# Performance work log

Hardware: AMD Instinct MI355X
Metric: run time of the kernel (lower is better)

## Reference

```python
import jax, jax.numpy as jnp
import numpy as np

N = 50000      # nodes
E = 1600000    # edges (avg degree 32)
D_IN = 128
H = 256        # 2 * out_channels
D_OUT = 128
NEG_SLOPE = 0.2


def setup_inputs() -> dict:
    key = jax.random.key(0)
    ks = jax.random.split(key, 16)
    x = jax.random.normal(ks[0], (N, D_IN), dtype=jnp.float32)
    edge_index = jax.random.randint(ks[1], (2, E), 0, N, dtype=jnp.int64)

    def lin(k, fan_in, fan_out):
        s = 1.0 / np.sqrt(fan_in)
        return jax.random.uniform(k, (fan_in, fan_out), jnp.float32, -s, s)

    def att(k, d):
        s = 1.0 / np.sqrt(d)
        return jax.random.uniform(k, (d,), jnp.float32, -s, s)

    return {
        "x": x, "edge_index": edge_index,
        "W1": lin(ks[2], D_IN, H), "a1_src": att(ks[3], H), "a1_dst": att(ks[4], H), "b1": jnp.zeros((H,), jnp.float32),
        "W2": lin(ks[5], H, H),    "a2_src": att(ks[6], H), "a2_dst": att(ks[7], H), "b2": jnp.zeros((H,), jnp.float32),
        "W3": lin(ks[8], H, D_OUT),"a3_src": att(ks[9], D_OUT), "a3_dst": att(ks[10], D_OUT), "b3": jnp.zeros((D_OUT,), jnp.float32),
    }


def _gat_conv(x, W, a_src, a_dst, b, src, dst):
    # x: [N, Cin] -> h: [N, Cout]
    h = x @ W
    # per-node attention logits, gathered along edges (edge j->i: src=j, dst=i)
    e = jax.nn.leaky_relu((h @ a_src)[src] + (h @ a_dst)[dst], NEG_SLOPE)  # [E]
    # segment softmax over incoming edges of each destination node
    m = jax.ops.segment_max(e, dst, num_segments=N)          # [N]
    p = jnp.exp(e - m[dst])                                  # [E]
    denom = jax.ops.segment_sum(p, dst, num_segments=N)      # [N]
    alpha = p / denom[dst]                                   # [E]
    # scatter-add weighted source features
    out = jax.ops.segment_sum(alpha[:, None] * h[src], dst, num_segments=N)
    return out + b


def reference(x, edge_index, W1, a1_src, a1_dst, b1, W2, a2_src, a2_dst, b2, W3, a3_src, a3_dst, b3):
    src, dst = edge_index[0], edge_index[1]
    h = jax.nn.relu(_gat_conv(x, W1, a1_src, a1_dst, b1, src, dst))
    for _ in range(2):  # hidden_layers, shared conv2 weights
        h = jax.nn.relu(_gat_conv(h, W2, a2_src, a2_dst, b2, src, dst))
    out = _gat_conv(h, W3, a3_src, a3_dst, b3, src, dst)
    return jax.nn.softmax(out, axis=1)
```

## Files before the change

kernel.cpp:

```cpp
#include <hip/hip_runtime.h>
#include <hip/hip_bf16.h>
#include <hip/hip_fp16.h>

#define NN 50000
#define EE 1600000
#define DIN 128
#define HH 256
#define DOUT 128

typedef __attribute__((ext_vector_type(8))) short short8;
typedef __attribute__((ext_vector_type(4))) float f32x4;

__device__ __forceinline__ short f2bf(float v) {
    union { float f; unsigned u; } a;
    a.f = v;
    unsigned r = a.u + 0x7fffu + ((a.u >> 16) & 1u);
    return (short)(r >> 16);
}
__device__ __forceinline__ float bf2f(short h) {
    union { unsigned u; float f; } a;
    a.u = ((unsigned)(unsigned short)h) << 16;
    return a.f;
}


__global__ __launch_bounds__(256) void hist_kernel(const int* __restrict__ dst, int* __restrict__ deg, int E) {
    int e = blockIdx.x * 256 + threadIdx.x;
    if (e < E) atomicAdd(&deg[dst[e]], 1);
}

#define SCAN_B 256

__global__ __launch_bounds__(SCAN_B) void scan1_kernel(const int* __restrict__ deg, int* __restrict__ exc,
                                                       int* __restrict__ bsum, int n) {
    __shared__ int tmp[SCAN_B];
    int i = blockIdx.x * SCAN_B + threadIdx.x;
    int v = (i < n) ? deg[i] : 0;
    tmp[threadIdx.x] = v;
    __syncthreads();
    for (int o = 1; o < SCAN_B; o <<= 1) {
        int t = (threadIdx.x >= o) ? tmp[threadIdx.x - o] : 0;
        __syncthreads();
        tmp[threadIdx.x] += t;
        __syncthreads();
    }
    if (i < n) exc[i] = tmp[threadIdx.x] - v;
    if (threadIdx.x == SCAN_B - 1) bsum[blockIdx.x] = tmp[SCAN_B - 1];
}

__global__ __launch_bounds__(SCAN_B) void scan2_kernel(int* __restrict__ bsum, int nb) {
    __shared__ int tmp[SCAN_B];
    int v = (threadIdx.x < nb) ? bsum[threadIdx.x] : 0;
    tmp[threadIdx.x] = v;
    __syncthreads();
    for (int o = 1; o < SCAN_B; o <<= 1) {
        int t = (threadIdx.x >= o) ? tmp[threadIdx.x - o] : 0;
        __syncthreads();
        tmp[threadIdx.x] += t;
        __syncthreads();
    }
    if (threadIdx.x < nb) bsum[threadIdx.x] = tmp[threadIdx.x] - v;
}

__global__ __launch_bounds__(SCAN_B) void scan3_kernel(int* __restrict__ exc, const int* __restrict__ bsum,
                                                       int* __restrict__ cursor, int n, int E) {
    int i = blockIdx.x * SCAN_B + threadIdx.x;
    if (i < n) {
        int v = exc[i] + bsum[blockIdx.x];
        exc[i] = v;
        cursor[i] = v;
    }
    if (i == n) exc[n] = E;
}

#define NCB 256

__global__ __launch_bounds__(256) void scatter8_kernel(const int* __restrict__ src, const int* __restrict__ dst,
                                                       int* __restrict__ cursor, int* __restrict__ es, int E, int n) {
    int q = blockIdx.x & 7;
    int cb = blockIdx.x >> 3;
    int lo = q * (n >> 3);
    int hi = (q == 7) ? n : lo + (n >> 3);
    int chunk = (E + NCB - 1) / NCB;
    int e1 = min((cb + 1) * chunk, E);
    for (int e = cb * chunk + threadIdx.x; e < e1; e += 256) {
        int d = dst[e];
        if (d >= lo && d < hi) {
            int pos = atomicAdd(&cursor[d], 1);
            es[pos] = src[e];
        }
    }
}


__global__ __launch_bounds__(256) void wsplit_kernel(const float* __restrict__ W, short* __restrict__ WhT,
                                                     short* __restrict__ WlT, int K, int C) {
    int f = blockIdx.x * 256 + threadIdx.x;
    if (f >= K * C) return;
    int k = f / C, c = f % C;
    float v = W[f];
    short h = f2bf(v);
    short l = f2bf(v - bf2f(h));
    WhT[(size_t)c * K + k] = h;
    WlT[(size_t)c * K + k] = l;
}


__global__ __launch_bounds__(256) void tohalf_kernel(const float* __restrict__ in, __half* __restrict__ out,
                                                     size_t cnt) {
    size_t i = (size_t)(blockIdx.x * 256 + threadIdx.x) * 4;
    if (i + 3 < cnt) {
        float4 v = *(const float4*)(in + i);
        __half h0 = __float2half(v.x), h1 = __float2half(v.y);
        __half h2 = __float2half(v.z), h3 = __float2half(v.w);
        __half2* op = (__half2*)(out + i);
        op[0] = __half2(h0, h1);
        op[1] = __half2(h2, h3);
    }
}


template <bool BRELU, bool DOTS, bool HOUT>
__global__ __launch_bounds__(256) void gemm_mfma_kernel(const float* __restrict__ X, const short* __restrict__ BhT,
                                                        const short* __restrict__ BlT, const float* __restrict__ bias,
                                                        float* __restrict__ out, const float* __restrict__ a1v,
                                                        const float* __restrict__ a2v, float* __restrict__ s1,
                                                        float* __restrict__ s2, int n, int K, int Cout) {
    __shared__ short Ah[128][40], Al[128][40];
    __shared__ short Bh[128][40], Bl[128][40];
    int tid = threadIdx.x;
    int row0 = blockIdx.y * 128, col0 = blockIdx.x * 128;
    int lane = tid & 63, wid = tid >> 6;
    int wr = (wid >> 1) * 64, wc = (wid & 1) * 64;

    f32x4 acc[4][4];
#pragma unroll
    for (int mi = 0; mi < 4; ++mi)
#pragma unroll
        for (int ni = 0; ni < 4; ++ni) acc[mi][ni] = 0.f;

    int srow = tid >> 1;
    int sk = (tid & 1) * 16;

    for (int k0 = 0; k0 < K; k0 += 32) {
        {
            float v[16];
            int gr = row0 + srow;
            if (gr < n) {
                const float* p = X + (size_t)gr * K + k0 + sk;
                float4 f0 = ((const float4*)p)[0];
                float4 f1 = ((const float4*)p)[1];
                float4 f2 = ((const float4*)p)[2];
                float4 f3 = ((const float4*)p)[3];
                v[0] = f0.x; v[1] = f0.y; v[2] = f0.z; v[3] = f0.w;
                v[4] = f1.x; v[5] = f1.y; v[6] = f1.z; v[7] = f1.w;
                v[8] = f2.x; v[9] = f2.y; v[10] = f2.z; v[11] = f2.w;
                v[12] = f3.x; v[13] = f3.y; v[14] = f3.z; v[15] = f3.w;
            } else {
#pragma unroll
                for (int j = 0; j < 16; ++j) v[j] = 0.f;
            }
            short8 h0, h1, l0, l1;
#pragma unroll
            for (int j = 0; j < 8; ++j) {
                short h = f2bf(v[j]);
                h0[j] = h;
                l0[j] = f2bf(v[j] - bf2f(h));
            }
#pragma unroll
            for (int j = 0; j < 8; ++j) {
                short h = f2bf(v[8 + j]);
                h1[j] = h;
                l1[j] = f2bf(v[8 + j] - bf2f(h));
            }
            *(short8*)&Ah[srow][sk] = h0;
            *(short8*)&Ah[srow][sk + 8] = h1;
            *(short8*)&Al[srow][sk] = l0;
            *(short8*)&Al[srow][sk + 8] = l1;
        }
        {
            const short* ph = BhT + (size_t)(col0 + srow) * K + k0 + sk;
            const short* pl = BlT + (size_t)(col0 + srow) * K + k0 + sk;
            short8 bh0 = ((const short8*)ph)[0];
            short8 bh1 = ((const short8*)ph)[1];
            short8 bl0 = ((const short8*)pl)[0];
            short8 bl1 = ((const short8*)pl)[1];
            *(short8*)&Bh[srow][sk] = bh0;
            *(short8*)&Bh[srow][sk + 8] = bh1;
            *(short8*)&Bl[srow][sk] = bl0;
            *(short8*)&Bl[srow][sk + 8] = bl1;
        }
        __syncthreads();

        int fr = lane & 15, kb = lane >> 4;
        short8 a_h[4], a_l[4];
#pragma unroll
        for (int mi = 0; mi < 4; ++mi) {
            a_h[mi] = *(const short8*)&Ah[wr + mi * 16 + fr][kb * 8];
            a_l[mi] = *(const short8*)&Al[wr + mi * 16 + fr][kb * 8];
        }
#pragma unroll
        for (int ni = 0; ni < 4; ++ni) {
            short8 b_h = *(const short8*)&Bh[wc + ni * 16 + fr][kb * 8];
            short8 b_l = *(const short8*)&Bl[wc + ni * 16 + fr][kb * 8];
#pragma unroll
            for (int mi = 0; mi < 4; ++mi) {
                acc[mi][ni] = __builtin_amdgcn_mfma_f32_16x16x32_bf16(a_l[mi], b_h, acc[mi][ni], 0, 0, 0);
                acc[mi][ni] = __builtin_amdgcn_mfma_f32_16x16x32_bf16(a_h[mi], b_l, acc[mi][ni], 0, 0, 0);
                acc[mi][ni] = __builtin_amdgcn_mfma_f32_16x16x32_bf16(a_h[mi], b_h, acc[mi][ni], 0, 0, 0);
            }
        }
        __syncthreads();
    }

    int dc = lane & 15, dr = (lane >> 4) * 4;

    if (DOTS) {
#pragma unroll
        for (int mi = 0; mi < 4; ++mi) {
#pragma unroll
            for (int r = 0; r < 4; ++r) {
                float p1 = 0.f, p2 = 0.f;
#pragma unroll
                for (int ni = 0; ni < 4; ++ni) {
                    int gcol = col0 + wc + ni * 16 + dc;
                    float v = acc[mi][ni][r];
                    p1 = fmaf(v, a1v[gcol], p1);
                    p2 = fmaf(v, a2v[gcol], p2);
                }
#pragma unroll
                for (int o = 8; o; o >>= 1) {
                    p1 += __shfl_xor(p1, o, 64);
                    p2 += __shfl_xor(p2, o, 64);
                }
                int grow = row0 + wr + mi * 16 + dr + r;
                if (dc == 0 && grow < n) {
                    atomicAdd(s1 + grow, p1);
                    atomicAdd(s2 + grow, p2);
                }
            }
        }
    }

#pragma unroll
    for (int mi = 0; mi < 4; ++mi) {
#pragma unroll
        for (int r = 0; r < 4; ++r) {
            int grow = row0 + wr + mi * 16 + dr + r;
            if (grow >= n) continue;
#pragma unroll
            for (int ni = 0; ni < 4; ++ni) {
                int gcol = col0 + wc + ni * 16 + dc;
                float v = acc[mi][ni][r];
                if (BRELU) {
                    v += bias[gcol];
                    v = fmaxf(v, 0.f);
                }
                if (HOUT) {
                    ((__half*)out)[(size_t)grow * Cout + gcol] = __float2half(v);
                } else {
                    out[(size_t)grow * Cout + gcol] = v;
                }
            }
        }
    }
}


__global__ __launch_bounds__(256) void rowdots_kernel(const float* __restrict__ H, const float* __restrict__ a1,
                                                      const float* __restrict__ a2, float* __restrict__ s1,
                                                      float* __restrict__ s2, int n, int C) {
    int w = (blockIdx.x * 256 + threadIdx.x) >> 6;
    int lane = threadIdx.x & 63;
    if (w >= n) return;
    const float* hp = H + (size_t)w * C;
    float acc1 = 0.f, acc2 = 0.f;
    for (int c = lane; c < C; c += 64) {
        float hv = hp[c];
        acc1 = fmaf(hv, a1[c], acc1);
        acc2 = fmaf(hv, a2[c], acc2);
    }
#pragma unroll
    for (int o = 32; o; o >>= 1) {
        acc1 += __shfl_xor(acc1, o, 64);
        acc2 += __shfl_xor(acc2, o, 64);
    }
    if (lane == 0) {
        s1[w] = acc1;
        s2[w] = acc2;
    }
}


template <int C, bool RELU, bool SOFTMAX>
__global__ __launch_bounds__(256) void aggf_kernel(const __half* __restrict__ H, const float* __restrict__ ssrc,
                                                   const float* __restrict__ sdst, const int* __restrict__ off,
                                                   const int* __restrict__ es, const float* __restrict__ bias,
                                                   float* __restrict__ out, int n) {
    constexpr int VPL = C / 64;
    int wid = threadIdx.x >> 6, lane = threadIdx.x & 63;
    int node = blockIdx.x * 4 + wid;
    if (node >= n) return;
    int beg = off[node], end = off[node + 1];
    float sd = sdst[node];

    float m = -3e38f;
    for (int e = beg + lane; e < end; e += 64) {
        float g = ssrc[es[e]] + sd;
        g = (g > 0.f) ? g : 0.2f * g;
        m = fmaxf(m, g);
    }
#pragma unroll
    for (int o = 32; o; o >>= 1) m = fmaxf(m, __shfl_xor(m, o, 64));

    float acc[VPL];
#pragma unroll
    for (int v = 0; v < VPL; ++v) acc[v] = 0.f;
    float den = 0.f;
    int c0 = lane * VPL;

    for (int base = beg; base < end; base += 64) {
        int e = base + lane;
        float p = 0.f;
        int s = 0;
        if (e < end) {
            s = es[e];
            float g = ssrc[s] + sd;
            g = (g > 0.f) ? g : 0.2f * g;
            p = __expf(g - m);
            den += p;
        }
        int cnt = end - base;
        if (cnt > 64) cnt = 64;
        int j0 = 0;
        for (; j0 + 8 <= cnt; j0 += 8) {
            float pj[8];
            const __half* hp[8];
#pragma unroll
            for (int u = 0; u < 8; ++u) {
                pj[u] = __shfl(p, j0 + u, 64);
                int sj = __shfl(s, j0 + u, 64);
                hp[u] = H + (size_t)sj * C + c0;
            }
            if (VPL == 4) {
                uint2 raw[8];
#pragma unroll
                for (int u = 0; u < 8; ++u) raw[u] = *(const uint2*)hp[u];
#pragma unroll
                for (int u = 0; u < 8; ++u) {
                    union { unsigned u32; __half2 h2; } lo, hi;
                    lo.u32 = raw[u].x;
                    hi.u32 = raw[u].y;
                    float2 f0 = __half22float2(lo.h2);
                    float2 f1 = __half22float2(hi.h2);
                    acc[0] = fmaf(pj[u], f0.x, acc[0]);
                    acc[1] = fmaf(pj[u], f0.y, acc[1]);
                    acc[2] = fmaf(pj[u], f1.x, acc[2]);
                    acc[3] = fmaf(pj[u], f1.y, acc[3]);
                }
            } else {
                __half2 hv[8];
#pragma unroll
                for (int u = 0; u < 8; ++u) hv[u] = *(const __half2*)hp[u];
#pragma unroll
                for (int u = 0; u < 8; ++u) {
                    float2 f = __half22float2(hv[u]);
                    acc[0] = fmaf(pj[u], f.x, acc[0]);
                    acc[1] = fmaf(pj[u], f.y, acc[1]);
                }
            }
        }
        for (; j0 < cnt; ++j0) {
            float pj = __shfl(p, j0, 64);
            int sj = __shfl(s, j0, 64);
            const __half* hp = H + (size_t)sj * C + c0;
            if (VPL == 4) {
                uint2 raw = *(const uint2*)hp;
                union { unsigned u32; __half2 h2; } lo, hi;
                lo.u32 = raw.x;
                hi.u32 = raw.y;
                float2 f0 = __half22float2(lo.h2);
                float2 f1 = __half22float2(hi.h2);
                acc[0] = fmaf(pj, f0.x, acc[0]);
                acc[1] = fmaf(pj, f0.y, acc[1]);
                acc[2] = fmaf(pj, f1.x, acc[2]);
                acc[3] = fmaf(pj, f1.y, acc[3]);
            } else {
                float2 f = __half22float2(*(const __half2*)hp);
                acc[0] = fmaf(pj, f.x, acc[0]);
                acc[1] = fmaf(pj, f.y, acc[1]);
            }
        }
    }

#pragma unroll
    for (int o = 32; o; o >>= 1) den += __shfl_xor(den, o, 64);
    float inv = (den > 0.f) ? 1.f / den : 0.f;

    float ov[VPL];
#pragma unroll
    for (int v = 0; v < VPL; ++v) {
        float bb = bias ? bias[c0 + v] : 0.f;
        ov[v] = fmaf(acc[v], inv, bb);
        if (RELU) ov[v] = fmaxf(ov[v], 0.f);
    }
    if (SOFTMAX) {
        float mm = ov[0];
#pragma unroll
        for (int v = 1; v < VPL; ++v) mm = fmaxf(mm, ov[v]);
#pragma unroll
        for (int o = 32; o; o >>= 1) mm = fmaxf(mm, __shfl_xor(mm, o, 64));
        float ss = 0.f;
#pragma unroll
        for (int v = 0; v < VPL; ++v) {
            ov[v] = __expf(ov[v] - mm);
            ss += ov[v];
        }
#pragma unroll
        for (int o = 32; o; o >>= 1) ss += __shfl_xor(ss, o, 64);
        float si = 1.f / ss;
#pragma unroll
        for (int v = 0; v < VPL; ++v) ov[v] *= si;
    }
    float* op = out + (size_t)node * C + c0;
    if (VPL == 4)
        *(float4*)op = make_float4(ov[0], ov[1], ov[2], ov[3]);
    else
        *(float2*)op = make_float2(ov[0], ov[1]);
}


extern "C" void kernel_launch(void* const* d_in, const int* in_sizes, int n_in,
                              void* d_out, int out_size, void* d_ws, size_t ws_size,
                              hipStream_t stream) {
    const float* x = (const float*)d_in[0];
    const int* ei = (const int*)d_in[1];
    const float* W1 = (const float*)d_in[2];
    const float* a1s = (const float*)d_in[3];
    const float* a1d = (const float*)d_in[4];
    const float* b1 = (const float*)d_in[5];
    const float* W2 = (const float*)d_in[6];
    const float* a2s = (const float*)d_in[7];
    const float* a2d = (const float*)d_in[8];
    const float* b2 = (const float*)d_in[9];
    const float* W3 = (const float*)d_in[10];
    const float* a3s = (const float*)d_in[11];
    const float* a3d = (const float*)d_in[12];
    const float* b3 = (const float*)d_in[13];

    const int n = NN, E = EE;
    const int* src = ei;
    const int* dst = ei + E;

    char* base = (char*)d_ws;
    size_t o = 0;
    auto alloc = [&](size_t bytes) -> char* {
        char* p = base + o;
        o += (bytes + 255) & ~(size_t)255;
        return p;
    };
    int* off = (int*)alloc((n + 1) * sizeof(int));
    int* cur = (int*)alloc((n + 1) * sizeof(int));
    int* bsum = (int*)alloc(1024 * sizeof(int));
    int* es = (int*)alloc((size_t)E * sizeof(int));
    float* sbuf = (float*)alloc((size_t)2 * n * sizeof(float));
    float* ssrc = sbuf;
    float* sdst = sbuf + n;
    float* was = (float*)alloc(256 * sizeof(float));
    float* wad = (float*)alloc(256 * sizeof(float));
    short* W1h = (short*)alloc((size_t)DIN * HH * sizeof(short));
    short* W1l = (short*)alloc((size_t)DIN * HH * sizeof(short));
    short* W2h = (short*)alloc((size_t)HH * HH * sizeof(short));
    short* W2l = (short*)alloc((size_t)HH * HH * sizeof(short));
    short* W3h = (short*)alloc((size_t)HH * DOUT * sizeof(short));
    short* W3l = (short*)alloc((size_t)HH * DOUT * sizeof(short));
    __half* xh = (__half*)alloc((size_t)n * DIN * sizeof(__half));
    __half* Hh = (__half*)alloc((size_t)n * HH * sizeof(__half));
    float* Hbuf = (float*)alloc((size_t)n * HH * sizeof(float));
    float* Abuf = (float*)alloc((size_t)n * HH * sizeof(float));
    (void)ws_size;

    hipMemsetAsync(cur, 0, (n + 1) * sizeof(int), stream);
    hist_kernel<<<(E + 255) / 256, 256, 0, stream>>>(dst, cur, E);
    int nb = (n + SCAN_B - 1) / SCAN_B;
    scan1_kernel<<<nb, SCAN_B, 0, stream>>>(cur, off, bsum, n);
    scan2_kernel<<<1, SCAN_B, 0, stream>>>(bsum, nb);
    scan3_kernel<<<nb, SCAN_B, 0, stream>>>(off, bsum, cur, n, E);
    scatter8_kernel<<<NCB * 8, 256, 0, stream>>>(src, dst, cur, es, E, n);

    wsplit_kernel<<<(DIN * HH + 255) / 256, 256, 0, stream>>>(W1, W1h, W1l, DIN, HH);
    wsplit_kernel<<<(HH * HH + 255) / 256, 256, 0, stream>>>(W2, W2h, W2l, HH, HH);
    wsplit_kernel<<<(HH * DOUT + 255) / 256, 256, 0, stream>>>(W3, W3h, W3l, HH, DOUT);
    tohalf_kernel<<<((n * DIN / 4) + 255) / 256, 256, 0, stream>>>(x, xh, (size_t)n * DIN);

    int wgrid = (n * 64 + 255) / 256;
    int agrid = (n + 3) / 4;
    int rb = (n + 127) / 128;

    {
        rowdots_kernel<<<(128 * 64 + 255) / 256, 256, 0, stream>>>(W1, a1s, a1d, was, wad, DIN, HH);
        rowdots_kernel<<<wgrid, 256, 0, stream>>>(x, was, wad, ssrc, sdst, n, DIN);
        aggf_kernel<DIN, false, false><<<agrid, 256, 0, stream>>>(xh, ssrc, sdst, off, es, nullptr, Hbuf, n);
        dim3 g(HH / 128, rb);
        gemm_mfma_kernel<true, false, false><<<g, 256, 0, stream>>>(Hbuf, W1h, W1l, b1, Abuf, nullptr, nullptr,
                                                                    nullptr, nullptr, n, DIN, HH);
    }
    for (int t = 0; t < 2; ++t) {
        dim3 g(HH / 128, rb);
        hipMemsetAsync(sbuf, 0, (size_t)2 * n * sizeof(float), stream);
        gemm_mfma_kernel<false, true, true><<<g, 256, 0, stream>>>(Abuf, W2h, W2l, nullptr, (float*)Hh, a2s, a2d,
                                                                   ssrc, sdst, n, HH, HH);
        aggf_kernel<HH, true, false><<<agrid, 256, 0, stream>>>(Hh, ssrc, sdst, off, es, b2, Abuf, n);
    }
    {
        dim3 g(DOUT / 128, rb);
        hipMemsetAsync(sbuf, 0, (size_t)2 * n * sizeof(float), stream);
        gemm_mfma_kernel<false, true, true><<<g, 256, 0, stream>>>(Abuf, W3h, W3l, nullptr, (float*)Hh, a3s, a3d,
                                                                   ssrc, sdst, n, HH, DOUT);
        aggf_kernel<DOUT, false, true><<<agrid, 256, 0, stream>>>(Hh, ssrc, sdst, off, es, b3, (float*)d_out, n);
    }
}
```

Before: 665.5 us.

## Use 16-byte half loads with multi-edge lane groups in aggregation

Rewrites the GAT aggregation kernel so each lane loads 8 half values (16 bytes) per edge, with lane groups in a wavefront handling several edges at once. Partial accumulators are combined with cross-lane shuffles before normalization, and only one group writes the output. This aims to cut the number of gather memory instructions and raise memory-level parallelism. In exchange it adds a shuffle reduction and per-lane register use.

```diff
diff --git a/kernel.cpp b/kernel.cpp
--- a/kernel.cpp
+++ b/kernel.cpp
@@ -292,32 +292,54 @@
 }
 
 
+__device__ __forceinline__ void fma8(const uint4& raw, float pj, float* acc) {
+    union { unsigned u; __half2 h; } w;
+    w.u = raw.x;
+    float2 f = __half22float2(w.h);
+    acc[0] = fmaf(pj, f.x, acc[0]);
+    acc[1] = fmaf(pj, f.y, acc[1]);
+    w.u = raw.y;
+    f = __half22float2(w.h);
+    acc[2] = fmaf(pj, f.x, acc[2]);
+    acc[3] = fmaf(pj, f.y, acc[3]);
+    w.u = raw.z;
+    f = __half22float2(w.h);
+    acc[4] = fmaf(pj, f.x, acc[4]);
+    acc[5] = fmaf(pj, f.y, acc[5]);
+    w.u = raw.w;
+    f = __half22float2(w.h);
+    acc[6] = fmaf(pj, f.x, acc[6]);
+    acc[7] = fmaf(pj, f.y, acc[7]);
+}
+
 template <int C, bool RELU, bool SOFTMAX>
-__global__ __launch_bounds__(256) void aggf_kernel(const __half* __restrict__ H, const float* __restrict__ ssrc,
-                                                   const float* __restrict__ sdst, const int* __restrict__ off,
-                                                   const int* __restrict__ es, const float* __restrict__ bias,
-                                                   float* __restrict__ out, int n) {
-    constexpr int VPL = C / 64;
+__global__ __launch_bounds__(256) void agg16_kernel(const __half* __restrict__ H, const float* __restrict__ ssrc,
+                                                    const float* __restrict__ sdst, const int* __restrict__ off,
+                                                    const int* __restrict__ es, const float* __restrict__ bias,
+                                                    float* __restrict__ out, int n) {
+    constexpr int GE = 512 / C;
+    constexpr int LPR = 64 / GE;
     int wid = threadIdx.x >> 6, lane = threadIdx.x & 63;
     int node = blockIdx.x * 4 + wid;
     if (node >= n) return;
     int beg = off[node], end = off[node + 1];
     float sd = sdst[node];
+    int g = lane / LPR;
+    int c0 = (lane % LPR) * 8;
 
     float m = -3e38f;
     for (int e = beg + lane; e < end; e += 64) {
-        float g = ssrc[es[e]] + sd;
-        g = (g > 0.f) ? g : 0.2f * g;
-        m = fmaxf(m, g);
+        float v = ssrc[es[e]] + sd;
+        v = (v > 0.f) ? v : 0.2f * v;
+        m = fmaxf(m, v);
     }
 #pragma unroll
     for (int o = 32; o; o >>= 1) m = fmaxf(m, __shfl_xor(m, o, 64));
 
-    float acc[VPL];
-#pragma unroll
-    for (int v = 0; v < VPL; ++v) acc[v] = 0.f;
+    float acc[8];
+#pragma unroll
+    for (int v = 0; v < 8; ++v) acc[v] = 0.f;
     float den = 0.f;
-    int c0 = lane * VPL;
 
     for (int base = beg; base < end; base += 64) {
         int e = base + lane;
@@ -325,81 +347,56 @@
         int s = 0;
         if (e < end) {
             s = es[e];
-            float g = ssrc[s] + sd;
-            g = (g > 0.f) ? g : 0.2f * g;
-            p = __expf(g - m);
+            float v = ssrc[s] + sd;
+            v = (v > 0.f) ? v : 0.2f * v;
+            p = __expf(v - m);
             den += p;
         }
         int cnt = end - base;
         if (cnt > 64) cnt = 64;
         int j0 = 0;
-        for (; j0 + 8 <= cnt; j0 += 8) {
+        for (; j0 + 8 * GE <= cnt; j0 += 8 * GE) {
             float pj[8];
-            const __half* hp[8];
+            const uint4* hp[8];
 #pragma unroll
             for (int u = 0; u < 8; ++u) {
-                pj[u] = __shfl(p, j0 + u, 64);
-                int sj = __shfl(s, j0 + u, 64);
-                hp[u] = H + (size_t)sj * C + c0;
-            }
-            if (VPL == 4) {
-                uint2 raw[8];
-#pragma unroll
-                for (int u = 0; u < 8; ++u) raw[u] = *(const uint2*)hp[u];
-#pragma unroll
-                for (int u = 0; u < 8; ++u) {
-                    union { unsigned u32; __half2 h2; } lo, hi;
-                    lo.u32 = raw[u].x;
-                    hi.u32 = raw[u].y;
-                    float2 f0 = __half22float2(lo.h2);
-                    float2 f1 = __half22float2(hi.h2);
-                    acc[0] = fmaf(pj[u], f0.x, acc[0]);
-                    acc[1] = fmaf(pj[u], f0.y, acc[1]);
-                    acc[2] = fmaf(pj[u], f1.x, acc[2]);
-                    acc[3] = fmaf(pj[u], f1.y, acc[3]);
-                }
-            } else {
-                __half2 hv[8];
-#pragma unroll
-                for (int u = 0; u < 8; ++u) hv[u] = *(const __half2*)hp[u];
-#pragma unroll
-                for (int u = 0; u < 8; ++u) {
-                    float2 f = __half22float2(hv[u]);
-                    acc[0] = fmaf(pj[u], f.x, acc[0]);
-                    acc[1] = fmaf(pj[u], f.y, acc[1]);
-                }
-            }
-        }
-        for (; j0 < cnt; ++j0) {
-            float pj = __shfl(p, j0, 64);
-            int sj = __shfl(s, j0, 64);
-            const __half* hp = H + (size_t)sj * C + c0;
-            if (VPL == 4) {
-                uint2 raw = *(const uint2*)hp;
-                union { unsigned u32; __half2 h2; } lo, hi;
-                lo.u32 = raw.x;
-                hi.u32 = raw.y;
-                float2 f0 = __half22float2(lo.h2);
-                float2 f1 = __half22float2(hi.h2);
-                acc[0] = fmaf(pj, f0.x, acc[0]);
-                acc[1] = fmaf(pj, f0.y, acc[1]);
-                acc[2] = fmaf(pj, f1.x, acc[2]);
-                acc[3] = fmaf(pj, f1.y, acc[3]);
-            } else {
-                float2 f = __half22float2(*(const __half2*)hp);
-                acc[0] = fmaf(pj, f.x, acc[0]);
-                acc[1] = fmaf(pj, f.y, acc[1]);
-            }
-        }
-    }
+                int j = j0 + u * GE + g;
+                pj[u] = __shfl(p, j, 64);
+                int sj = __shfl(s, j, 64);
+                hp[u] = (const uint4*)(H + (size_t)sj * C + c0);
+            }
+            uint4 raw[8];
+#pragma unroll
+            for (int u = 0; u < 8; ++u) raw[u] = *hp[u];
+#pragma unroll
+            for (int u = 0; u < 8; ++u) fma8(raw[u], pj[u], acc);
+        }
+        for (; j0 < cnt; j0 += GE) {
+            int j = j0 + g;
+            bool ok = j < cnt;
+            int jj = ok ? j : cnt - 1;
+            float pj = __shfl(p, jj, 64);
+            if (!ok) pj = 0.f;
+            int sj = __shfl(s, jj, 64);
+            uint4 raw = *(const uint4*)(H + (size_t)sj * C + c0);
+            fma8(raw, pj, acc);
+        }
+    }
+
+    if (GE == 4) {
+#pragma unroll
+        for (int v = 0; v < 8; ++v) acc[v] += __shfl_xor(acc[v], 16, 64);
+    }
+#pragma unroll
+    for (int v = 0; v < 8; ++v) acc[v] += __shfl_xor(acc[v], 32, 64);
 
 #pragma unroll
     for (int o = 32; o; o >>= 1) den += __shfl_xor(den, o, 64);
     float inv = (den > 0.f) ? 1.f / den : 0.f;
 
-    float ov[VPL];
-#pragma unroll
-    for (int v = 0; v < VPL; ++v) {
+    float ov[8];
+#pragma unroll
+    for (int v = 0; v < 8; ++v) {
         float bb = bias ? bias[c0 + v] : 0.f;
         ov[v] = fmaf(acc[v], inv, bb);
         if (RELU) ov[v] = fmaxf(ov[v], 0.f);
@@ -407,26 +404,26 @@
     if (SOFTMAX) {
         float mm = ov[0];
 #pragma unroll
-        for (int v = 1; v < VPL; ++v) mm = fmaxf(mm, ov[v]);
-#pragma unroll
-        for (int o = 32; o; o >>= 1) mm = fmaxf(mm, __shfl_xor(mm, o, 64));
+        for (int v = 1; v < 8; ++v) mm = fmaxf(mm, ov[v]);
+#pragma unroll
+        for (int o = 8; o; o >>= 1) mm = fmaxf(mm, __shfl_xor(mm, o, 64));
         float ss = 0.f;
 #pragma unroll
-        for (int v = 0; v < VPL; ++v) {
+        for (int v = 0; v < 8; ++v) {
             ov[v] = __expf(ov[v] - mm);
             ss += ov[v];
         }
 #pragma unroll
-        for (int o = 32; o; o >>= 1) ss += __shfl_xor(ss, o, 64);
+        for (int o = 8; o; o >>= 1) ss += __shfl_xor(ss, o, 64);
         float si = 1.f / ss;
 #pragma unroll
-        for (int v = 0; v < VPL; ++v) ov[v] *= si;
-    }
-    float* op = out + (size_t)node * C + c0;
-    if (VPL == 4)
+        for (int v = 0; v < 8; ++v) ov[v] *= si;
+    }
+    if (g == 0) {
+        float* op = out + (size_t)node * C + c0;
         *(float4*)op = make_float4(ov[0], ov[1], ov[2], ov[3]);
-    else
-        *(float2*)op = make_float2(ov[0], ov[1]);
+        *(float4*)(op + 4) = make_float4(ov[4], ov[5], ov[6], ov[7]);
+    }
 }
 
 
@@ -500,7 +497,7 @@
     {
         rowdots_kernel<<<(128 * 64 + 255) / 256, 256, 0, stream>>>(W1, a1s, a1d, was, wad, DIN, HH);
         rowdots_kernel<<<wgrid, 256, 0, stream>>>(x, was, wad, ssrc, sdst, n, DIN);
-        aggf_kernel<DIN, false, false><<<agrid, 256, 0, stream>>>(xh, ssrc, sdst, off, es, nullptr, Hbuf, n);
+        agg16_kernel<DIN, false, false><<<agrid, 256, 0, stream>>>(xh, ssrc, sdst, off, es, nullptr, Hbuf, n);
         dim3 g(HH / 128, rb);
         gemm_mfma_kernel<true, false, false><<<g, 256, 0, stream>>>(Hbuf, W1h, W1l, b1, Abuf, nullptr, nullptr,
                                                                     nullptr, nullptr, n, DIN, HH);
@@ -510,13 +507,13 @@
         hipMemsetAsync(sbuf, 0, (size_t)2 * n * sizeof(float), stream);
         gemm_mfma_kernel<false, true, true><<<g, 256, 0, stream>>>(Abuf, W2h, W2l, nullptr, (float*)Hh, a2s, a2d,
                                                                    ssrc, sdst, n, HH, HH);
-        aggf_kernel<HH, true, false><<<agrid, 256, 0, stream>>>(Hh, ssrc, sdst, off, es, b2, Abuf, n);
+        agg16_kernel<HH, true, false><<<agrid, 256, 0, stream>>>(Hh, ssrc, sdst, off, es, b2, Abuf, n);
     }
     {
         dim3 g(DOUT / 128, rb);
         hipMemsetAsync(sbuf, 0, (size_t)2 * n * sizeof(float), stream);
         gemm_mfma_kernel<false, true, true><<<g, 256, 0, stream>>>(Abuf, W3h, W3l, nullptr, (float*)Hh, a3s, a3d,
                                                                    ssrc, sdst, n, HH, DOUT);
-        aggf_kernel<DOUT, false, true><<<agrid, 256, 0, stream>>>(Hh, ssrc, sdst, off, es, b3, (float*)d_out, n);
-    }
-}
+        agg16_kernel<DOUT, false, true><<<agrid, 256, 0, stream>>>(Hh, ssrc, sdst, off, es, b3, (float*)d_out, n);
+    }
+}
```

Measured after the change: 748.6 us. 12.5% more time.
